# Kernel optimization log

Measured on AMD Instinct MI355X. Metric: run time of the kernel, lower is better.

The kernel has to match this reference:

```python
import jax, jax.numpy as jnp
import numpy as np

B, L, K = 16384, 512, 4
N_ITERS = 5
EPS = 1e-08
NOISE_SCALE = 0.01


def setup_inputs() -> dict:
    key = jax.random.key(0)
    k1, k2, k3 = jax.random.split(key, 3)
    return {
        "windows": jax.random.normal(k1, (B, L), dtype=jnp.float32),
        "init_centers": jax.random.normal(k2, (K,), dtype=jnp.float32),
        "init_scales": jnp.ones((K,), dtype=jnp.float32),
        "init_weights": jnp.ones((K,), dtype=jnp.float32) / K,
        "prior_p_param": -jnp.ones((1,), dtype=jnp.float32),
        "weights_param": jnp.zeros((1, L), dtype=jnp.float32),
        "blend": jnp.zeros((1,), dtype=jnp.float32),
        "noise": jax.random.normal(k3, (B, K), dtype=jnp.float32),
    }


def _em(windows, init_centers, init_scales, init_weights,
        prior_p_param, weights_param, blend, noise):
    # windows: [B, L]
    data_mean = jnp.mean(windows, axis=-1, keepdims=True)          # [B, 1]
    data_std = jnp.std(windows, axis=-1, keepdims=True, ddof=1)    # [B, 1] (torch.std is unbiased)
    prior_var = jnp.var(windows, axis=-1, keepdims=True, ddof=1)   # [B, 1]

    # _initialize_parameters (noise passed in as standard normal, scaled here)
    mu = init_centers[None, :] * data_std + data_mean + noise * data_std * NOISE_SCALE  # [B, K]
    sigma = jnp.abs(init_scales)[None, :] * data_std                                    # [B, K]
    w = jnp.broadcast_to(init_weights[None, :], mu.shape)                               # [B, K]

    # _get_parameters
    weights = jnp.exp(weights_param)[..., None]   # [1, L, 1]
    blender = jax.nn.sigmoid(blend)               # [1]
    prior_p = jax.nn.sigmoid(prior_p_param)       # [1]

    g = None
    for _ in range(N_ITERS):
        # E-step: responsibilities via stable softmax over components
        log_w = jnp.log((w + EPS) / (sigma + EPS))[:, None, :]                 # [B, 1, K]
        z = (windows[..., None] - mu[:, None, :]) / (sigma[:, None, :] + EPS)  # [B, L, K]
        log_mix = -0.5 * z * z + log_w                                         # [B, L, K]
        g = jax.nn.softmax(log_mix, axis=-1)                                   # [B, L, K]

        # M-step
        wg = g * weights                                   # [B, L, K]
        sum_g = jnp.maximum(jnp.sum(wg, axis=-2), EPS)     # [B, K]
        w = sum_g + prior_p
        w = w / jnp.sum(w, axis=-1, keepdims=True)
        data_mu = jnp.sum(wg * windows[..., None], axis=-2) / sum_g            # [B, K]
        mu = data_mu * blender + data_mean * (1.0 - blender)                   # [B, K]
        diff = windows[..., None] - mu[:, None, :]                             # [B, L, K]
        data_var = jnp.sum(wg * diff * diff, axis=-2) / sum_g                  # [B, K]
        var = data_var * blender + prior_var * (1.0 - blender)
        sigma = jnp.sqrt(var + EPS)

    return g, w, mu, sigma


def reference(windows, init_centers, init_scales, init_weights,
              prior_p_param, weights_param, blend, noise):
    return _em(windows, init_centers, init_scales, init_weights,
               prior_p_param, weights_param, blend, noise)
```

## Files before the change

### kernel.cpp

```cpp
#include <hip/hip_runtime.h>
#include <math.h>


constexpr int Bn = 16384;
constexpr int Ln = 512;
constexpr int Kn = 4;
constexpr int NITER = 5;
constexpr float EPSf = 1e-8f;
constexpr float NOISEf = 0.01f;
constexpr float LOG2E = 1.4426950408889634f;

__device__ __forceinline__ float frcp(float v) { return __builtin_amdgcn_rcpf(v); }
__device__ __forceinline__ float fexp2(float v) { return __builtin_amdgcn_exp2f(v); }

__device__ __forceinline__ float rlane(float v, int l) {
    return __int_as_float(__builtin_amdgcn_readlane(__float_as_int(v), l));
}

template <int CTRL>
__device__ __forceinline__ float dpp_mov(float v) {
    return __int_as_float(
        __builtin_amdgcn_update_dpp(0, __float_as_int(v), CTRL, 0xF, 0xF, true));
}
template <int CTRL>
__device__ __forceinline__ float dpp_add(float v) {
    return v + dpp_mov<CTRL>(v);
}

#define WRED3_STEP(ctrl) \
    "v_add_f32_dpp %0, %0, %0 " ctrl " row_mask:0xf bank_mask:0xf bound_ctrl:0\n\t" \
    "v_add_f32_dpp %1, %1, %1 " ctrl " row_mask:0xf bank_mask:0xf bound_ctrl:0\n\t" \
    "v_add_f32_dpp %2, %2, %2 " ctrl " row_mask:0xf bank_mask:0xf bound_ctrl:0\n\t"

__device__ __forceinline__ void wred3(float& a, float& b, float& c) {
    asm volatile(
        "s_nop 1\n\t"
        WRED3_STEP("row_shr:1")
        WRED3_STEP("row_shr:2")
        WRED3_STEP("row_shr:4")
        WRED3_STEP("row_shr:8")
        WRED3_STEP("row_bcast:15")
        WRED3_STEP("row_bcast:31")
        "s_nop 1"
        : "+v"(a), "+v"(b), "+v"(c));
}

struct RowState {
    float x[8], xx[8], wl[8];
    float muk, wk, invsek, sigk;
    float mean, prior_var, blender, prior_p;
    float bm, bv;
    float W0, W1, W2;
};

template <bool LAST>
__device__ __forceinline__ void em_iter(RowState& st, float* __restrict__ gp0,
                                        int kk) {
    float is2 = st.invsek * st.invsek;
    float lw2 = __log2f((st.wk + EPSf) * st.invsek);
    float Ak = (-0.5f * LOG2E) * is2;
    float Bk = (LOG2E * st.muk) * is2;
    float Ck = fmaf((-0.5f * LOG2E) * (st.muk * st.muk), is2, lw2);
    float dAl = Ak - dpp_mov<0xFF>(Ak);
    float dBl = Bk - dpp_mov<0xFF>(Bk);
    float dCl = Ck - dpp_mov<0xFF>(Ck);
    float a0 = rlane(dAl, 0), a1 = rlane(dAl, 1), a2 = rlane(dAl, 2);
    float b0 = rlane(dBl, 0), b1 = rlane(dBl, 1), b2 = rlane(dBl, 2);
    float c0 = rlane(dCl, 0), c1 = rlane(dCl, 1), c2 = rlane(dCl, 2);

    float S00 = 0, S01 = 0, S02 = 0;
    float S10 = 0, S11 = 0, S12 = 0;
    float S20 = 0, S21 = 0, S22 = 0;
#pragma unroll
    for (int j = 0; j < 8; ++j) {
        float lm0 = fmaf(a0, st.xx[j], fmaf(b0, st.x[j], c0));
        float lm1 = fmaf(a1, st.xx[j], fmaf(b1, st.x[j], c1));
        float lm2 = fmaf(a2, st.xx[j], fmaf(b2, st.x[j], c2));
        float r0 = fexp2(lm0);
        float r1 = fexp2(lm1);
        float r2 = fexp2(lm2);
        float esum = (r0 + r1) + (r2 + 1.f);
        float inv = frcp(esum);
        float wls = st.wl[j] * inv;
        float wlsx = wls * st.x[j];
        float wlsxx = wls * st.xx[j];
        S00 = fmaf(r0, wls, S00); S10 = fmaf(r0, wlsx, S10); S20 = fmaf(r0, wlsxx, S20);
        S01 = fmaf(r1, wls, S01); S11 = fmaf(r1, wlsx, S11); S21 = fmaf(r1, wlsxx, S21);
        S02 = fmaf(r2, wls, S02); S12 = fmaf(r2, wlsx, S12); S22 = fmaf(r2, wlsxx, S22);
        if (LAST) {
            float4 g4 = make_float4(r0 * inv, r1 * inv, r2 * inv, inv);
            if (j < 4) *(float4*)(gp0 + 4 * j) = g4;
            else       *(float4*)(gp0 + 1024 + 4 * (j - 4)) = g4;
        }
    }

    wred3(S00, S10, S20);
    wred3(S01, S11, S21);
    wred3(S02, S12, S22);
    float s00 = rlane(S00, 63), s10 = rlane(S10, 63), s20 = rlane(S20, 63);
    float s01 = rlane(S01, 63), s11 = rlane(S11, 63), s21 = rlane(S21, 63);
    float s02 = rlane(S02, 63), s12 = rlane(S12, 63), s22 = rlane(S22, 63);
    float d0 = st.W0 - s00 - s01 - s02;
    float d1 = st.W1 - s10 - s11 - s12;
    float d2 = st.W2 - s20 - s21 - s22;
    float vT0 = (kk == 0) ? s00 : (kk == 1) ? s01 : (kk == 2) ? s02 : d0;
    float vT1 = (kk == 0) ? s10 : (kk == 1) ? s11 : (kk == 2) ? s12 : d1;
    float vT2 = (kk == 0) ? s20 : (kk == 1) ? s21 : (kk == 2) ? s22 : d2;

    float sg = fmaxf(vT0, EPSf);
    float rsg = frcp(sg);
    float mun = fmaf(st.blender, vT1 * rsg, st.bm);
    float num = fmaf(mun * mun, vT0, fmaf(-2.f * mun, vT1, vT2));
    float dv = fmaxf(num * rsg, 0.f);
    float var = fmaf(st.blender, dv, st.bv);
    float sgn = sqrtf(var + EPSf);
    st.muk = mun;
    st.sigk = sgn;
    st.invsek = frcp(sgn + EPSf);
    float wn = sg + st.prior_p;
    float ws = dpp_add<0xB1>(wn);
    ws = dpp_add<0x4E>(ws);
    st.wk = wn * frcp(ws);
}

__global__ __launch_bounds__(256, 8) void em_kernel(
    const float* __restrict__ windows,
    const float* __restrict__ centers,
    const float* __restrict__ scales,
    const float* __restrict__ iweights,
    const float* __restrict__ prior_p_param,
    const float* __restrict__ weights_param,
    const float* __restrict__ blend,
    const float* __restrict__ noise,
    float* __restrict__ out_g,
    float* __restrict__ out_w,
    float* __restrict__ out_mu,
    float* __restrict__ out_sigma)
{
    const int lane = threadIdx.x & 63;
    const int kk = lane & 3;
    const int b = blockIdx.x * 4 + (threadIdx.x >> 6);

    RowState st;
    const float* __restrict__ xr = windows + (size_t)b * Ln;
    const float4 q0 = *(const float4*)(xr + 4 * lane);
    const float4 q1 = *(const float4*)(xr + 256 + 4 * lane);
    st.x[0] = q0.x; st.x[1] = q0.y; st.x[2] = q0.z; st.x[3] = q0.w;
    st.x[4] = q1.x; st.x[5] = q1.y; st.x[6] = q1.z; st.x[7] = q1.w;

    const float4 e0 = *(const float4*)(weights_param + 4 * lane);
    const float4 e1 = *(const float4*)(weights_param + 256 + 4 * lane);
    st.wl[0] = __expf(e0.x); st.wl[1] = __expf(e0.y);
    st.wl[2] = __expf(e0.z); st.wl[3] = __expf(e0.w);
    st.wl[4] = __expf(e1.x); st.wl[5] = __expf(e1.y);
    st.wl[6] = __expf(e1.z); st.wl[7] = __expf(e1.w);

    float s = 0.f, ss = 0.f, w0 = 0.f, w1 = 0.f, w2 = 0.f;
#pragma unroll
    for (int j = 0; j < 8; ++j) {
        st.xx[j] = st.x[j] * st.x[j];
        s += st.x[j];
        ss += st.xx[j];
        w0 += st.wl[j];
        w1 = fmaf(st.wl[j], st.x[j], w1);
        w2 = fmaf(st.wl[j], st.xx[j], w2);
    }
    float junk = 0.f;
    wred3(s, ss, w0);
    wred3(w1, w2, junk);
    s = rlane(s, 63);
    ss = rlane(ss, 63);
    st.W0 = rlane(w0, 63);
    st.W1 = rlane(w1, 63);
    st.W2 = rlane(w2, 63);

    st.mean = s * (1.0f / Ln);
    float var1 = fmaxf((ss - s * st.mean) * (1.0f / (Ln - 1)), 0.f);
    const float sd = sqrtf(var1);
    st.prior_var = var1;

    st.prior_p = 1.f / (1.f + __expf(-prior_p_param[0]));
    st.blender = 1.f / (1.f + __expf(-blend[0]));
    const float omb = 1.f - st.blender;
    st.bm = omb * st.mean;
    st.bv = omb * st.prior_var;

    st.muk = fmaf(centers[kk], sd, st.mean) + noise[(size_t)b * 4 + kk] * sd * NOISEf;
    float sg0 = fabsf(scales[kk]) * sd;
    st.sigk = sg0;
    st.wk = iweights[kk];
    st.invsek = frcp(sg0 + EPSf);

    float* gp0 = out_g + (size_t)b * (Ln * Kn) + 16 * lane;

    for (int it = 0; it < NITER - 1; ++it)
        em_iter<false>(st, gp0, kk);
    em_iter<true>(st, gp0, kk);

    if (lane < 4) {
        out_w[(size_t)b * 4 + lane]     = st.wk;
        out_mu[(size_t)b * 4 + lane]    = st.muk;
        out_sigma[(size_t)b * 4 + lane] = st.sigk;
    }
}

extern "C" void kernel_launch(void* const* d_in, const int* in_sizes, int n_in,
                              void* d_out, int out_size, void* d_ws, size_t ws_size,
                              hipStream_t stream) {
    const float* windows       = (const float*)d_in[0];
    const float* init_centers  = (const float*)d_in[1];
    const float* init_scales   = (const float*)d_in[2];
    const float* init_weights  = (const float*)d_in[3];
    const float* prior_p_param = (const float*)d_in[4];
    const float* weights_param = (const float*)d_in[5];
    const float* blend         = (const float*)d_in[6];
    const float* noise         = (const float*)d_in[7];

    float* out       = (float*)d_out;
    float* out_g     = out;
    float* out_w     = out_g + (size_t)Bn * Ln * Kn;
    float* out_mu    = out_w + (size_t)Bn * Kn;
    float* out_sigma = out_mu + (size_t)Bn * Kn;

    dim3 grid(Bn / 4);
    dim3 block(256);
    hipLaunchKernelGGL(em_kernel, grid, block, 0, stream,
                       windows, init_centers, init_scales, init_weights,
                       prior_p_param, weights_param, blend, noise,
                       out_g, out_w, out_mu, out_sigma);
}
```

Before: 217.3 us.

## Process two rows per wavefront with interleaved EM iterations and batched reductions

Each wavefront now runs the EM loop on two adjacent rows at once. The exp2, rcp and accumulation chains of both rows are interleaved, and their DPP cross-lane reductions are merged into six-wide batches, so serial latency is hidden by independent work. The exp of weights_param and the W0 sum are computed once and shared by both rows. The grid is halved and launch bounds drop from 8 to 4 blocks per CU. This trades lower occupancy and higher register pressure for more instruction-level parallelism.

```diff
diff --git a/kernel.cpp b/kernel.cpp
--- a/kernel.cpp
+++ b/kernel.cpp
@@ -45,85 +45,156 @@
         : "+v"(a), "+v"(b), "+v"(c));
 }
 
-struct RowState {
-    float x[8], xx[8], wl[8];
+#define WRED6_STEP(ctrl) \
+    "v_add_f32_dpp %0, %0, %0 " ctrl " row_mask:0xf bank_mask:0xf bound_ctrl:0\n\t" \
+    "v_add_f32_dpp %1, %1, %1 " ctrl " row_mask:0xf bank_mask:0xf bound_ctrl:0\n\t" \
+    "v_add_f32_dpp %2, %2, %2 " ctrl " row_mask:0xf bank_mask:0xf bound_ctrl:0\n\t" \
+    "v_add_f32_dpp %3, %3, %3 " ctrl " row_mask:0xf bank_mask:0xf bound_ctrl:0\n\t" \
+    "v_add_f32_dpp %4, %4, %4 " ctrl " row_mask:0xf bank_mask:0xf bound_ctrl:0\n\t" \
+    "v_add_f32_dpp %5, %5, %5 " ctrl " row_mask:0xf bank_mask:0xf bound_ctrl:0\n\t"
+
+__device__ __forceinline__ void wred6(float& a, float& b, float& c,
+                                      float& d, float& e, float& f) {
+    asm volatile(
+        "s_nop 1\n\t"
+        WRED6_STEP("row_shr:1")
+        WRED6_STEP("row_shr:2")
+        WRED6_STEP("row_shr:4")
+        WRED6_STEP("row_shr:8")
+        WRED6_STEP("row_bcast:15")
+        WRED6_STEP("row_bcast:31")
+        "s_nop 1"
+        : "+v"(a), "+v"(b), "+v"(c), "+v"(d), "+v"(e), "+v"(f));
+}
+
+struct Row {
+    float x[8], xx[8];
     float muk, wk, invsek, sigk;
-    float mean, prior_var, blender, prior_p;
+    float W1, W2;
     float bm, bv;
-    float W0, W1, W2;
 };
 
-template <bool LAST>
-__device__ __forceinline__ void em_iter(RowState& st, float* __restrict__ gp0,
-                                        int kk) {
-    float is2 = st.invsek * st.invsek;
-    float lw2 = __log2f((st.wk + EPSf) * st.invsek);
+__device__ __forceinline__ void coeffs(const Row& R,
+        float& a0, float& a1, float& a2,
+        float& b0, float& b1, float& b2,
+        float& c0, float& c1, float& c2) {
+    float is2 = R.invsek * R.invsek;
+    float lw2 = __log2f((R.wk + EPSf) * R.invsek);
     float Ak = (-0.5f * LOG2E) * is2;
-    float Bk = (LOG2E * st.muk) * is2;
-    float Ck = fmaf((-0.5f * LOG2E) * (st.muk * st.muk), is2, lw2);
+    float Bk = (LOG2E * R.muk) * is2;
+    float Ck = fmaf((-0.5f * LOG2E) * (R.muk * R.muk), is2, lw2);
     float dAl = Ak - dpp_mov<0xFF>(Ak);
     float dBl = Bk - dpp_mov<0xFF>(Bk);
     float dCl = Ck - dpp_mov<0xFF>(Ck);
-    float a0 = rlane(dAl, 0), a1 = rlane(dAl, 1), a2 = rlane(dAl, 2);
-    float b0 = rlane(dBl, 0), b1 = rlane(dBl, 1), b2 = rlane(dBl, 2);
-    float c0 = rlane(dCl, 0), c1 = rlane(dCl, 1), c2 = rlane(dCl, 2);
-
-    float S00 = 0, S01 = 0, S02 = 0;
-    float S10 = 0, S11 = 0, S12 = 0;
-    float S20 = 0, S21 = 0, S22 = 0;
-#pragma unroll
-    for (int j = 0; j < 8; ++j) {
-        float lm0 = fmaf(a0, st.xx[j], fmaf(b0, st.x[j], c0));
-        float lm1 = fmaf(a1, st.xx[j], fmaf(b1, st.x[j], c1));
-        float lm2 = fmaf(a2, st.xx[j], fmaf(b2, st.x[j], c2));
-        float r0 = fexp2(lm0);
-        float r1 = fexp2(lm1);
-        float r2 = fexp2(lm2);
-        float esum = (r0 + r1) + (r2 + 1.f);
-        float inv = frcp(esum);
-        float wls = st.wl[j] * inv;
-        float wlsx = wls * st.x[j];
-        float wlsxx = wls * st.xx[j];
-        S00 = fmaf(r0, wls, S00); S10 = fmaf(r0, wlsx, S10); S20 = fmaf(r0, wlsxx, S20);
-        S01 = fmaf(r1, wls, S01); S11 = fmaf(r1, wlsx, S11); S21 = fmaf(r1, wlsxx, S21);
-        S02 = fmaf(r2, wls, S02); S12 = fmaf(r2, wlsx, S12); S22 = fmaf(r2, wlsxx, S22);
-        if (LAST) {
-            float4 g4 = make_float4(r0 * inv, r1 * inv, r2 * inv, inv);
-            if (j < 4) *(float4*)(gp0 + 4 * j) = g4;
-            else       *(float4*)(gp0 + 1024 + 4 * (j - 4)) = g4;
-        }
-    }
-
-    wred3(S00, S10, S20);
-    wred3(S01, S11, S21);
-    wred3(S02, S12, S22);
-    float s00 = rlane(S00, 63), s10 = rlane(S10, 63), s20 = rlane(S20, 63);
-    float s01 = rlane(S01, 63), s11 = rlane(S11, 63), s21 = rlane(S21, 63);
-    float s02 = rlane(S02, 63), s12 = rlane(S12, 63), s22 = rlane(S22, 63);
-    float d0 = st.W0 - s00 - s01 - s02;
-    float d1 = st.W1 - s10 - s11 - s12;
-    float d2 = st.W2 - s20 - s21 - s22;
+    a0 = rlane(dAl, 0); a1 = rlane(dAl, 1); a2 = rlane(dAl, 2);
+    b0 = rlane(dBl, 0); b1 = rlane(dBl, 1); b2 = rlane(dBl, 2);
+    c0 = rlane(dCl, 0); c1 = rlane(dCl, 1); c2 = rlane(dCl, 2);
+}
+
+__device__ __forceinline__ void mstep(Row& R, float blender, float prior_p,
+        float W0,
+        float s00, float s01, float s02,
+        float s10, float s11, float s12,
+        float s20, float s21, float s22, int kk) {
+    float d0 = W0 - s00 - s01 - s02;
+    float d1 = R.W1 - s10 - s11 - s12;
+    float d2 = R.W2 - s20 - s21 - s22;
     float vT0 = (kk == 0) ? s00 : (kk == 1) ? s01 : (kk == 2) ? s02 : d0;
     float vT1 = (kk == 0) ? s10 : (kk == 1) ? s11 : (kk == 2) ? s12 : d1;
     float vT2 = (kk == 0) ? s20 : (kk == 1) ? s21 : (kk == 2) ? s22 : d2;
-
     float sg = fmaxf(vT0, EPSf);
     float rsg = frcp(sg);
-    float mun = fmaf(st.blender, vT1 * rsg, st.bm);
+    float mun = fmaf(blender, vT1 * rsg, R.bm);
     float num = fmaf(mun * mun, vT0, fmaf(-2.f * mun, vT1, vT2));
     float dv = fmaxf(num * rsg, 0.f);
-    float var = fmaf(st.blender, dv, st.bv);
+    float var = fmaf(blender, dv, R.bv);
     float sgn = sqrtf(var + EPSf);
-    st.muk = mun;
-    st.sigk = sgn;
-    st.invsek = frcp(sgn + EPSf);
-    float wn = sg + st.prior_p;
+    R.muk = mun;
+    R.sigk = sgn;
+    R.invsek = frcp(sgn + EPSf);
+    float wn = sg + prior_p;
     float ws = dpp_add<0xB1>(wn);
     ws = dpp_add<0x4E>(ws);
-    st.wk = wn * frcp(ws);
-}
-
-__global__ __launch_bounds__(256, 8) void em_kernel(
+    R.wk = wn * frcp(ws);
+}
+
+template <bool LAST>
+__device__ __forceinline__ void em_iter2(Row& A, Row& B, const float wl[8],
+        float W0, float blender, float prior_p,
+        float* __restrict__ gpA, float* __restrict__ gpB, int kk) {
+    float a0A, a1A, a2A, b0A, b1A, b2A, c0A, c1A, c2A;
+    float a0B, a1B, a2B, b0B, b1B, b2B, c0B, c1B, c2B;
+    coeffs(A, a0A, a1A, a2A, b0A, b1A, b2A, c0A, c1A, c2A);
+    coeffs(B, a0B, a1B, a2B, b0B, b1B, b2B, c0B, c1B, c2B);
+
+    float SA00 = 0, SA01 = 0, SA02 = 0, SA10 = 0, SA11 = 0, SA12 = 0,
+          SA20 = 0, SA21 = 0, SA22 = 0;
+    float SB00 = 0, SB01 = 0, SB02 = 0, SB10 = 0, SB11 = 0, SB12 = 0,
+          SB20 = 0, SB21 = 0, SB22 = 0;
+#pragma unroll
+    for (int j = 0; j < 8; ++j) {
+        float lmA0 = fmaf(a0A, A.xx[j], fmaf(b0A, A.x[j], c0A));
+        float lmA1 = fmaf(a1A, A.xx[j], fmaf(b1A, A.x[j], c1A));
+        float lmA2 = fmaf(a2A, A.xx[j], fmaf(b2A, A.x[j], c2A));
+        float rA0 = fexp2(lmA0);
+        float rA1 = fexp2(lmA1);
+        float rA2 = fexp2(lmA2);
+        float lmB0 = fmaf(a0B, B.xx[j], fmaf(b0B, B.x[j], c0B));
+        float lmB1 = fmaf(a1B, B.xx[j], fmaf(b1B, B.x[j], c1B));
+        float lmB2 = fmaf(a2B, B.xx[j], fmaf(b2B, B.x[j], c2B));
+        float rB0 = fexp2(lmB0);
+        float rB1 = fexp2(lmB1);
+        float rB2 = fexp2(lmB2);
+
+        float esA = (rA0 + rA1) + (rA2 + 1.f);
+        float invA = frcp(esA);
+        float esB = (rB0 + rB1) + (rB2 + 1.f);
+        float invB = frcp(esB);
+
+        float wlsA = wl[j] * invA;
+        float wlsxA = wlsA * A.x[j];
+        float wlsxxA = wlsA * A.xx[j];
+        SA00 = fmaf(rA0, wlsA, SA00); SA10 = fmaf(rA0, wlsxA, SA10); SA20 = fmaf(rA0, wlsxxA, SA20);
+        SA01 = fmaf(rA1, wlsA, SA01); SA11 = fmaf(rA1, wlsxA, SA11); SA21 = fmaf(rA1, wlsxxA, SA21);
+        SA02 = fmaf(rA2, wlsA, SA02); SA12 = fmaf(rA2, wlsxA, SA12); SA22 = fmaf(rA2, wlsxxA, SA22);
+
+        float wlsB = wl[j] * invB;
+        float wlsxB = wlsB * B.x[j];
+        float wlsxxB = wlsB * B.xx[j];
+        SB00 = fmaf(rB0, wlsB, SB00); SB10 = fmaf(rB0, wlsxB, SB10); SB20 = fmaf(rB0, wlsxxB, SB20);
+        SB01 = fmaf(rB1, wlsB, SB01); SB11 = fmaf(rB1, wlsxB, SB11); SB21 = fmaf(rB1, wlsxxB, SB21);
+        SB02 = fmaf(rB2, wlsB, SB02); SB12 = fmaf(rB2, wlsxB, SB12); SB22 = fmaf(rB2, wlsxxB, SB22);
+
+        if (LAST) {
+            float4 gA = make_float4(rA0 * invA, rA1 * invA, rA2 * invA, invA);
+            float4 gB = make_float4(rB0 * invB, rB1 * invB, rB2 * invB, invB);
+            if (j < 4) {
+                *(float4*)(gpA + 4 * j) = gA;
+                *(float4*)(gpB + 4 * j) = gB;
+            } else {
+                *(float4*)(gpA + 1024 + 4 * (j - 4)) = gA;
+                *(float4*)(gpB + 1024 + 4 * (j - 4)) = gB;
+            }
+        }
+    }
+
+    wred6(SA00, SA10, SA20, SB00, SB10, SB20);
+    wred6(SA01, SA11, SA21, SB01, SB11, SB21);
+    wred6(SA02, SA12, SA22, SB02, SB12, SB22);
+    float sA00 = rlane(SA00, 63), sA10 = rlane(SA10, 63), sA20 = rlane(SA20, 63);
+    float sA01 = rlane(SA01, 63), sA11 = rlane(SA11, 63), sA21 = rlane(SA21, 63);
+    float sA02 = rlane(SA02, 63), sA12 = rlane(SA12, 63), sA22 = rlane(SA22, 63);
+    float sB00 = rlane(SB00, 63), sB10 = rlane(SB10, 63), sB20 = rlane(SB20, 63);
+    float sB01 = rlane(SB01, 63), sB11 = rlane(SB11, 63), sB21 = rlane(SB21, 63);
+    float sB02 = rlane(SB02, 63), sB12 = rlane(SB12, 63), sB22 = rlane(SB22, 63);
+
+    mstep(A, blender, prior_p, W0, sA00, sA01, sA02, sA10, sA11, sA12,
+          sA20, sA21, sA22, kk);
+    mstep(B, blender, prior_p, W0, sB00, sB01, sB02, sB10, sB11, sB12,
+          sB20, sB21, sB22, kk);
+}
+
+__global__ __launch_bounds__(256, 4) void em_kernel(
     const float* __restrict__ windows,
     const float* __restrict__ centers,
     const float* __restrict__ scales,
@@ -139,68 +210,87 @@
 {
     const int lane = threadIdx.x & 63;
     const int kk = lane & 3;
-    const int b = blockIdx.x * 4 + (threadIdx.x >> 6);
-
-    RowState st;
-    const float* __restrict__ xr = windows + (size_t)b * Ln;
-    const float4 q0 = *(const float4*)(xr + 4 * lane);
-    const float4 q1 = *(const float4*)(xr + 256 + 4 * lane);
-    st.x[0] = q0.x; st.x[1] = q0.y; st.x[2] = q0.z; st.x[3] = q0.w;
-    st.x[4] = q1.x; st.x[5] = q1.y; st.x[6] = q1.z; st.x[7] = q1.w;
-
-    const float4 e0 = *(const float4*)(weights_param + 4 * lane);
-    const float4 e1 = *(const float4*)(weights_param + 256 + 4 * lane);
-    st.wl[0] = __expf(e0.x); st.wl[1] = __expf(e0.y);
-    st.wl[2] = __expf(e0.z); st.wl[3] = __expf(e0.w);
-    st.wl[4] = __expf(e1.x); st.wl[5] = __expf(e1.y);
-    st.wl[6] = __expf(e1.z); st.wl[7] = __expf(e1.w);
-
-    float s = 0.f, ss = 0.f, w0 = 0.f, w1 = 0.f, w2 = 0.f;
+    const int b0 = blockIdx.x * 8 + (threadIdx.x >> 6) * 2;
+
+    float wl[8];
+    {
+        const float4 e0 = *(const float4*)(weights_param + 4 * lane);
+        const float4 e1 = *(const float4*)(weights_param + 256 + 4 * lane);
+        wl[0] = __expf(e0.x); wl[1] = __expf(e0.y);
+        wl[2] = __expf(e0.z); wl[3] = __expf(e0.w);
+        wl[4] = __expf(e1.x); wl[5] = __expf(e1.y);
+        wl[6] = __expf(e1.z); wl[7] = __expf(e1.w);
+    }
+
+    Row A, B;
+    {
+        const float* __restrict__ xa = windows + (size_t)b0 * Ln;
+        const float4 qa0 = *(const float4*)(xa + 4 * lane);
+        const float4 qa1 = *(const float4*)(xa + 256 + 4 * lane);
+        A.x[0] = qa0.x; A.x[1] = qa0.y; A.x[2] = qa0.z; A.x[3] = qa0.w;
+        A.x[4] = qa1.x; A.x[5] = qa1.y; A.x[6] = qa1.z; A.x[7] = qa1.w;
+        const float* __restrict__ xb = xa + Ln;
+        const float4 qb0 = *(const float4*)(xb + 4 * lane);
+        const float4 qb1 = *(const float4*)(xb + 256 + 4 * lane);
+        B.x[0] = qb0.x; B.x[1] = qb0.y; B.x[2] = qb0.z; B.x[3] = qb0.w;
+        B.x[4] = qb1.x; B.x[5] = qb1.y; B.x[6] = qb1.z; B.x[7] = qb1.w;
+    }
+
+    float sA = 0.f, ssA = 0.f, w1A = 0.f, w2A = 0.f;
+    float sB = 0.f, ssB = 0.f, w1B = 0.f, w2B = 0.f;
+    float w0 = 0.f;
 #pragma unroll
     for (int j = 0; j < 8; ++j) {
-        st.xx[j] = st.x[j] * st.x[j];
-        s += st.x[j];
-        ss += st.xx[j];
-        w0 += st.wl[j];
-        w1 = fmaf(st.wl[j], st.x[j], w1);
-        w2 = fmaf(st.wl[j], st.xx[j], w2);
-    }
-    float junk = 0.f;
-    wred3(s, ss, w0);
-    wred3(w1, w2, junk);
-    s = rlane(s, 63);
-    ss = rlane(ss, 63);
-    st.W0 = rlane(w0, 63);
-    st.W1 = rlane(w1, 63);
-    st.W2 = rlane(w2, 63);
-
-    st.mean = s * (1.0f / Ln);
-    float var1 = fmaxf((ss - s * st.mean) * (1.0f / (Ln - 1)), 0.f);
-    const float sd = sqrtf(var1);
-    st.prior_var = var1;
-
-    st.prior_p = 1.f / (1.f + __expf(-prior_p_param[0]));
-    st.blender = 1.f / (1.f + __expf(-blend[0]));
-    const float omb = 1.f - st.blender;
-    st.bm = omb * st.mean;
-    st.bv = omb * st.prior_var;
-
-    st.muk = fmaf(centers[kk], sd, st.mean) + noise[(size_t)b * 4 + kk] * sd * NOISEf;
-    float sg0 = fabsf(scales[kk]) * sd;
-    st.sigk = sg0;
-    st.wk = iweights[kk];
-    st.invsek = frcp(sg0 + EPSf);
-
-    float* gp0 = out_g + (size_t)b * (Ln * Kn) + 16 * lane;
+        A.xx[j] = A.x[j] * A.x[j];
+        B.xx[j] = B.x[j] * B.x[j];
+        sA += A.x[j];  ssA += A.xx[j];
+        sB += B.x[j];  ssB += B.xx[j];
+        w0 += wl[j];
+        w1A = fmaf(wl[j], A.x[j], w1A);  w2A = fmaf(wl[j], A.xx[j], w2A);
+        w1B = fmaf(wl[j], B.x[j], w1B);  w2B = fmaf(wl[j], B.xx[j], w2B);
+    }
+    wred6(sA, ssA, w1A, w2A, sB, ssB);
+    wred3(w1B, w2B, w0);
+    sA = rlane(sA, 63);  ssA = rlane(ssA, 63);
+    sB = rlane(sB, 63);  ssB = rlane(ssB, 63);
+    A.W1 = rlane(w1A, 63);  A.W2 = rlane(w2A, 63);
+    B.W1 = rlane(w1B, 63);  B.W2 = rlane(w2B, 63);
+    const float W0 = rlane(w0, 63);
+
+    const float prior_p = 1.f / (1.f + __expf(-prior_p_param[0]));
+    const float blender = 1.f / (1.f + __expf(-blend[0]));
+    const float omb = 1.f - blender;
+
+    const float meanA = sA * (1.0f / Ln);
+    const float varA = fmaxf((ssA - sA * meanA) * (1.0f / (Ln - 1)), 0.f);
+    const float sdA = sqrtf(varA);
+    A.bm = omb * meanA;
+    A.bv = omb * varA;
+    const float meanB = sB * (1.0f / Ln);
+    const float varB = fmaxf((ssB - sB * meanB) * (1.0f / (Ln - 1)), 0.f);
+    const float sdB = sqrtf(varB);
+    B.bm = omb * meanB;
+    B.bv = omb * varB;
+
+    const float ck = centers[kk], sck = fabsf(scales[kk]), iwk = iweights[kk];
+    A.muk = fmaf(ck, sdA, meanA) + noise[(size_t)b0 * 4 + kk] * sdA * NOISEf;
+    B.muk = fmaf(ck, sdB, meanB) + noise[(size_t)(b0 + 1) * 4 + kk] * sdB * NOISEf;
+    float sgA = sck * sdA, sgB = sck * sdB;
+    A.sigk = sgA;  A.wk = iwk;  A.invsek = frcp(sgA + EPSf);
+    B.sigk = sgB;  B.wk = iwk;  B.invsek = frcp(sgB + EPSf);
+
+    float* gpA = out_g + (size_t)b0 * (Ln * Kn) + 16 * lane;
+    float* gpB = gpA + Ln * Kn;
 
     for (int it = 0; it < NITER - 1; ++it)
-        em_iter<false>(st, gp0, kk);
-    em_iter<true>(st, gp0, kk);
-
-    if (lane < 4) {
-        out_w[(size_t)b * 4 + lane]     = st.wk;
-        out_mu[(size_t)b * 4 + lane]    = st.muk;
-        out_sigma[(size_t)b * 4 + lane] = st.sigk;
+        em_iter2<false>(A, B, wl, W0, blender, prior_p, gpA, gpB, kk);
+    em_iter2<true>(A, B, wl, W0, blender, prior_p, gpA, gpB, kk);
+
+    if (lane < 8) {
+        const size_t o = (size_t)b0 * 4 + lane;
+        out_w[o]     = (lane < 4) ? A.wk : B.wk;
+        out_mu[o]    = (lane < 4) ? A.muk : B.muk;
+        out_sigma[o] = (lane < 4) ? A.sigk : B.sigk;
     }
 }
 
@@ -222,7 +312,7 @@
     float* out_mu    = out_w + (size_t)Bn * Kn;
     float* out_sigma = out_mu + (size_t)Bn * Kn;
 
-    dim3 grid(Bn / 4);
+    dim3 grid(Bn / 8);
     dim3 block(256);
     hipLaunchKernelGGL(em_kernel, grid, block, 0, stream,
                        windows, init_centers, init_scales, init_weights,
```

After: 209.3 us. -3.7%, faster.
